# Kernel optimization log

Measured on AMD Instinct MI355X. Metric: run time of the kernel, lower is better.

The kernel has to match this reference:

```python
import jax, jax.numpy as jnp
import numpy as np

D_MODEL = 1024
N_HEADS = 16
HEAD_DIM = D_MODEL // N_HEADS


def setup_inputs() -> dict:
    key = jax.random.key(0)
    ks = jax.random.split(key, 10)
    B, NQ, S = 8, 64, 4096
    inv = 1.0 / np.sqrt(D_MODEL)
    inp = {
        "queries": jax.random.normal(ks[0], (B, NQ, D_MODEL), dtype=jnp.float32),
        "context": jax.random.normal(ks[1], (B, S, D_MODEL), dtype=jnp.float32),
        "wq": jax.random.normal(ks[2], (D_MODEL, D_MODEL), dtype=jnp.float32) * inv,
        "bq": jnp.zeros((D_MODEL,), dtype=jnp.float32),
        "wk": jax.random.normal(ks[3], (D_MODEL, D_MODEL), dtype=jnp.float32) * inv,
        "bk": jnp.zeros((D_MODEL,), dtype=jnp.float32),
        "wv": jax.random.normal(ks[4], (D_MODEL, D_MODEL), dtype=jnp.float32) * inv,
        "bv": jnp.zeros((D_MODEL,), dtype=jnp.float32),
        "wo": jax.random.normal(ks[5], (D_MODEL, D_MODEL), dtype=jnp.float32) * inv,
        "bo": jnp.zeros((D_MODEL,), dtype=jnp.float32),
    }
    return inp


def reference(queries, context, wq, bq, wk, bk, wv, bv, wo, bo):
    B, NQ, D = queries.shape
    S = context.shape[1]
    H, HD = N_HEADS, HEAD_DIM
    scale = HD ** -0.5
    # projections (x @ W^T + b, matching nn.Linear)
    q = queries @ wq.T + bq            # (B, NQ, D)
    k = context @ wk.T + bk            # (B, S, D)
    v = context @ wv.T + bv            # (B, S, D)
    q = q.reshape(B, NQ, H, HD).transpose(0, 2, 1, 3)  # (B, H, NQ, HD)
    k = k.reshape(B, S, H, HD).transpose(0, 2, 1, 3)   # (B, H, S, HD)
    v = v.reshape(B, S, H, HD).transpose(0, 2, 1, 3)   # (B, H, S, HD)
    attn = jnp.einsum('bhnd,bhsd->bhns', q, k) * scale
    attn = jax.nn.softmax(attn, axis=-1)
    # dropout is identity at eval / p=0
    out = jnp.einsum('bhns,bhsd->bhnd', attn, v)        # (B, H, NQ, HD)
    out = out.transpose(0, 2, 1, 3).reshape(B, NQ, D)   # (B, NQ, D)
    return out @ wo.T + bo
```

## Files before the change

### kernel.cpp

```cpp
#include <hip/hip_runtime.h>
#include <stdint.h>

#define BATCH   8
#define NQL     64
#define SLEN    4096
#define DMODEL  1024
#define NHEADS  16
#define HDIM    64

typedef float          f32x4  __attribute__((ext_vector_type(4)));
typedef __bf16         bf16x8 __attribute__((ext_vector_type(8)));
typedef unsigned int   u32x4  __attribute__((ext_vector_type(4)));
typedef unsigned short u16x4  __attribute__((ext_vector_type(4)));
typedef unsigned short u16x8  __attribute__((ext_vector_type(8)));

__device__ __forceinline__ unsigned short f2bf(float f) {
  unsigned int u = __builtin_bit_cast(unsigned int, f);
  u += 0x7FFFu + ((u >> 16) & 1u);
  return (unsigned short)(u >> 16);
}

__device__ __forceinline__ f32x4 mfma16(bf16x8 a, bf16x8 b, f32x4 c) {
  return __builtin_amdgcn_mfma_f32_16x16x32_bf16(a, b, c, 0, 0, 0);
}

__device__ __forceinline__ bf16x8 lds_frag(const char* p) {
  u32x4 v = *(const u32x4*)p;
  return __builtin_bit_cast(bf16x8, v);
}

__device__ __forceinline__ void gload_lds16(const void* g, void* l) {
  __builtin_amdgcn_global_load_lds((const __attribute__((address_space(1))) void*)g,
                                   (__attribute__((address_space(3))) void*)l, 16, 0, 0);
}

__global__ __launch_bounds__(256) void cvt_bf16_kernel(const float* __restrict__ in,
                                                       unsigned short* __restrict__ out,
                                                       int n8) {
  int i = blockIdx.x * 256 + threadIdx.x;
  if (i >= n8) return;
  const float4* p = (const float4*)in + (size_t)i * 2;
  float4 a = p[0], b = p[1];
  u16x8 o;
  o[0] = f2bf(a.x); o[1] = f2bf(a.y); o[2] = f2bf(a.z); o[3] = f2bf(a.w);
  o[4] = f2bf(b.x); o[5] = f2bf(b.y); o[6] = f2bf(b.z); o[7] = f2bf(b.w);
  *((u16x8*)out + i) = o;
}

template<int MODE>
__global__ __launch_bounds__(256)
void gemm_bt(const unsigned short* __restrict__ A, const unsigned short* __restrict__ Bw,
             const float* __restrict__ bias, void* __restrict__ Cout,
             int M, int N, int K) {
  __shared__ char lds[32768];
  char* ldsA = lds;
  char* ldsB = lds + 16384;

  const int tid  = threadIdx.x;
  const int wave = tid >> 6, lane = tid & 63;
  const int g    = lane >> 4, ln = lane & 15;
  const int nbn  = N >> 7;
  const int brow = (int)(blockIdx.x / nbn) << 7;
  const int bcol = (int)(blockIdx.x % nbn) << 7;
  const int wr   = wave >> 1, wc = wave & 1;

  f32x4 acc[4][4];
#pragma unroll
  for (int i = 0; i < 4; ++i)
#pragma unroll
    for (int j = 0; j < 4; ++j) acc[i][j] = (f32x4){0.f, 0.f, 0.f, 0.f};

  const int KT = K >> 6;
  const int srow = lane >> 3;
  const int srcs = (lane & 7) ^ (srow & 7);

  for (int kt = 0; kt < KT; ++kt) {
#pragma unroll
    for (int c = wave; c < 16; c += 4) {
      int row = (c << 3) + srow;
      const char* ga = (const char*)A + (((size_t)(brow + row) * K + (kt << 6) + (srcs << 3)) << 1);
      gload_lds16(ga, ldsA + (c << 10));
      const char* gb = (const char*)Bw + (((size_t)(bcol + row) * K + (kt << 6) + (srcs << 3)) << 1);
      gload_lds16(gb, ldsB + (c << 10));
    }
    asm volatile("s_waitcnt vmcnt(0)" ::: "memory");
    __syncthreads();

#pragma unroll
    for (int ks = 0; ks < 2; ++ks) {
      bf16x8 af[4], bfr[4];
      const int slot = ((ks << 2) + g) ^ (ln & 7);
#pragma unroll
      for (int mt = 0; mt < 4; ++mt) {
        int row = wr * 64 + mt * 16 + ln;
        af[mt] = lds_frag(ldsA + row * 128 + (slot << 4));
      }
#pragma unroll
      for (int nt = 0; nt < 4; ++nt) {
        int row = wc * 64 + nt * 16 + ln;
        bfr[nt] = lds_frag(ldsB + row * 128 + (slot << 4));
      }
#pragma unroll
      for (int mt = 0; mt < 4; ++mt)
#pragma unroll
        for (int nt = 0; nt < 4; ++nt)
          acc[mt][nt] = mfma16(af[mt], bfr[nt], acc[mt][nt]);
    }
    __syncthreads();
  }

#pragma unroll
  for (int mt = 0; mt < 4; ++mt) {
#pragma unroll
    for (int nt = 0; nt < 4; ++nt) {
      f32x4 v = acc[mt][nt];
      int r0 = brow + wr * 64 + mt * 16 + g * 4;
      int c  = bcol + wc * 64 + nt * 16 + ln;
      float bi = bias[c];
      if constexpr (MODE == 0) {
        unsigned short* Cb = (unsigned short*)Cout;
#pragma unroll
        for (int j = 0; j < 4; ++j) Cb[(size_t)(r0 + j) * N + c] = f2bf(v[j] + bi);
      } else if constexpr (MODE == 1) {
        float* Cf = (float*)Cout;
#pragma unroll
        for (int j = 0; j < 4; ++j) Cf[(size_t)(r0 + j) * N + c] = v[j] + bi;
      } else {
        u16x4 pk;
#pragma unroll
        for (int j = 0; j < 4; ++j) pk[j] = f2bf(v[j] + bi);
        size_t base = ((size_t)(r0 >> 12) * 1024 + c) * 4096 + (size_t)(r0 & 4095);
        *(u16x4*)((unsigned short*)Cout + base) = pk;
      }
    }
  }
}

__global__ __launch_bounds__(256)
void attn_kernel(const unsigned short* __restrict__ Qp,
                 const unsigned short* __restrict__ Kp,
                 const unsigned short* __restrict__ Vt,
                 unsigned short* __restrict__ Aout) {
  __shared__ char ldsKV[2][16384];
  __shared__ unsigned int plds[4 * 16 * 36];

  const int bh = blockIdx.x;
  const int b = bh >> 4, h = bh & 15;
  const int tid = threadIdx.x;
  const int wave = tid >> 6, lane = tid & 63;
  const int g = lane >> 4, ln = lane & 15;
  const int pbase = wave * 576 + ln * 36;
  const int srow = lane >> 3;
  const int srcs = (lane & 7) ^ (srow & 7);

  const unsigned short* qb =
      Qp + ((size_t)(b * 64 + wave * 16 + ln) * 1024) + h * 64 + g * 8;
  bf16x8 qf[2];
  qf[0] = __builtin_bit_cast(bf16x8, *(const u32x4*)qb);
  qf[1] = __builtin_bit_cast(bf16x8, *(const u32x4*)(qb + 32));

  f32x4 oacc[4];
#pragma unroll
  for (int i = 0; i < 4; ++i) oacc[i] = (f32x4){0.f, 0.f, 0.f, 0.f};
  float mrun = -1e30f, lrun = 0.f;

  auto stage = [&](int t, int buf) {
    int s0 = t << 6;
    char* bK = ldsKV[buf];
#pragma unroll
    for (int c4 = 0; c4 < 4; ++c4) {
      int c = wave * 4 + c4;
      int cc = c & 7;
      int row = (cc << 3) + srow;
      const char* gsrc;
      if (c < 8)
        gsrc = (const char*)Kp + (((size_t)((b << 12) + s0 + row) * 1024 + (h << 6) + (srcs << 3)) << 1);
      else
        gsrc = (const char*)Vt + (((size_t)((b << 10) + (h << 6) + row) * 4096 + s0 + (srcs << 3)) << 1);
      gload_lds16(gsrc, bK + ((c < 8) ? 0 : 8192) + (cc << 10));
    }
  };

  stage(0, 0);
  const int NT = SLEN / 64;
  for (int t = 0; t < NT; ++t) {
    asm volatile("s_waitcnt vmcnt(0)" ::: "memory");
    __syncthreads();
    if (t + 1 < NT) stage(t + 1, (t + 1) & 1);

    char* bufK = ldsKV[t & 1];
    char* bufV = bufK + 8192;

    f32x4 s4[4];
#pragma unroll
    for (int i = 0; i < 4; ++i) s4[i] = (f32x4){0.f, 0.f, 0.f, 0.f};
#pragma unroll
    for (int ks = 0; ks < 2; ++ks) {
      const int slot = ((ks << 2) + g) ^ (ln & 7);
#pragma unroll
      for (int mt = 0; mt < 4; ++mt) {
        int row = mt * 16 + ln;
        s4[mt] = mfma16(lds_frag(bufK + row * 128 + (slot << 4)), qf[ks], s4[mt]);
      }
    }

    float tmax = -1e30f;
#pragma unroll
    for (int mt = 0; mt < 4; ++mt)
#pragma unroll
      for (int j = 0; j < 4; ++j) {
        float sv = s4[mt][j] * 0.125f;
        s4[mt][j] = sv;
        tmax = fmaxf(tmax, sv);
      }
    tmax = fmaxf(tmax, __shfl_xor(tmax, 16));
    tmax = fmaxf(tmax, __shfl_xor(tmax, 32));
    float mnew = fmaxf(mrun, tmax);
    float factor = __expf(mrun - mnew);
    float psum = 0.f;
#pragma unroll
    for (int mt = 0; mt < 4; ++mt) {
      float p0 = __expf(s4[mt][0] - mnew);
      float p1 = __expf(s4[mt][1] - mnew);
      float p2 = __expf(s4[mt][2] - mnew);
      float p3 = __expf(s4[mt][3] - mnew);
      psum += (p0 + p1) + (p2 + p3);
      plds[pbase + mt * 8 + g * 2 + 0] = (unsigned)f2bf(p0) | ((unsigned)f2bf(p1) << 16);
      plds[pbase + mt * 8 + g * 2 + 1] = (unsigned)f2bf(p2) | ((unsigned)f2bf(p3) << 16);
    }
    psum += __shfl_xor(psum, 16);
    psum += __shfl_xor(psum, 32);
    lrun = lrun * factor + psum;
    mrun = mnew;

    float fj0 = __shfl(factor, g * 4 + 0);
    float fj1 = __shfl(factor, g * 4 + 1);
    float fj2 = __shfl(factor, g * 4 + 2);
    float fj3 = __shfl(factor, g * 4 + 3);
#pragma unroll
    for (int nt = 0; nt < 4; ++nt) {
      oacc[nt][0] *= fj0; oacc[nt][1] *= fj1; oacc[nt][2] *= fj2; oacc[nt][3] *= fj3;
    }

#pragma unroll
    for (int kt2 = 0; kt2 < 2; ++kt2) {
      u32x4 pv;
      int pidx = pbase + kt2 * 16 + g * 4;
      pv[0] = plds[pidx]; pv[1] = plds[pidx + 1]; pv[2] = plds[pidx + 2]; pv[3] = plds[pidx + 3];
      bf16x8 pa = __builtin_bit_cast(bf16x8, pv);
      const int slot = ((kt2 << 2) + g) ^ (ln & 7);
#pragma unroll
      for (int nt = 0; nt < 4; ++nt) {
        int row = nt * 16 + ln;
        oacc[nt] = mfma16(pa, lds_frag(bufV + row * 128 + (slot << 4)), oacc[nt]);
      }
    }
  }

  float l0 = __shfl(lrun, g * 4 + 0);
  float l1 = __shfl(lrun, g * 4 + 1);
  float l2 = __shfl(lrun, g * 4 + 2);
  float l3 = __shfl(lrun, g * 4 + 3);
  float r0 = 1.f / l0, r1 = 1.f / l1, r2 = 1.f / l2, r3 = 1.f / l3;
#pragma unroll
  for (int nt = 0; nt < 4; ++nt) {
    int col = h * 64 + nt * 16 + ln;
    size_t rbase = (size_t)(b * 64 + wave * 16 + g * 4) * 1024 + col;
    Aout[rbase + 0 * 1024] = f2bf(oacc[nt][0] * r0);
    Aout[rbase + 1 * 1024] = f2bf(oacc[nt][1] * r1);
    Aout[rbase + 2 * 1024] = f2bf(oacc[nt][2] * r2);
    Aout[rbase + 3 * 1024] = f2bf(oacc[nt][3] * r3);
  }
}

extern "C" void kernel_launch(void* const* d_in, const int* in_sizes, int n_in,
                              void* d_out, int out_size, void* d_ws, size_t ws_size,
                              hipStream_t stream) {
  const float* queries = (const float*)d_in[0];
  const float* context = (const float*)d_in[1];
  const float* wq = (const float*)d_in[2];
  const float* bq = (const float*)d_in[3];
  const float* wk = (const float*)d_in[4];
  const float* bk = (const float*)d_in[5];
  const float* wv = (const float*)d_in[6];
  const float* bv = (const float*)d_in[7];
  const float* wo = (const float*)d_in[8];
  const float* bo = (const float*)d_in[9];

  const size_t CTX_E = (size_t)BATCH * SLEN * DMODEL;
  const size_t QRY_E = (size_t)BATCH * NQL * DMODEL;
  const size_t W_E   = (size_t)DMODEL * DMODEL;

  char* ws = (char*)d_ws;
  size_t off = 0;
  auto alloc = [&](size_t bytes) {
    char* p = ws + off;
    off += (bytes + 255) & ~(size_t)255;
    return p;
  };
  unsigned short* ctx_bf = (unsigned short*)alloc(CTX_E * 2);
  unsigned short* q_bf   = (unsigned short*)alloc(QRY_E * 2);
  unsigned short* wq_bf  = (unsigned short*)alloc(W_E * 2);
  unsigned short* wk_bf  = (unsigned short*)alloc(W_E * 2);
  unsigned short* wv_bf  = (unsigned short*)alloc(W_E * 2);
  unsigned short* wo_bf  = (unsigned short*)alloc(W_E * 2);
  unsigned short* Qp     = (unsigned short*)alloc(QRY_E * 2);
  unsigned short* Kp     = (unsigned short*)alloc(CTX_E * 2);
  unsigned short* Vt     = (unsigned short*)alloc(CTX_E * 2);
  unsigned short* Ao     = (unsigned short*)alloc(QRY_E * 2);
  if (off > ws_size) return;

  cvt_bf16_kernel<<<dim3((int)(CTX_E / 8 / 256)), 256, 0, stream>>>(context, ctx_bf, (int)(CTX_E / 8));
  cvt_bf16_kernel<<<dim3((int)(QRY_E / 8 / 256)), 256, 0, stream>>>(queries, q_bf, (int)(QRY_E / 8));
  cvt_bf16_kernel<<<dim3((int)(W_E / 8 / 256)), 256, 0, stream>>>(wq, wq_bf, (int)(W_E / 8));
  cvt_bf16_kernel<<<dim3((int)(W_E / 8 / 256)), 256, 0, stream>>>(wk, wk_bf, (int)(W_E / 8));
  cvt_bf16_kernel<<<dim3((int)(W_E / 8 / 256)), 256, 0, stream>>>(wv, wv_bf, (int)(W_E / 8));
  cvt_bf16_kernel<<<dim3((int)(W_E / 8 / 256)), 256, 0, stream>>>(wo, wo_bf, (int)(W_E / 8));

  const int M_KV = BATCH * SLEN;
  const int M_Q  = BATCH * NQL;

  gemm_bt<0><<<dim3((M_KV / 128) * (DMODEL / 128)), 256, 0, stream>>>(ctx_bf, wk_bf, bk, Kp, M_KV, DMODEL, DMODEL);
  gemm_bt<2><<<dim3((M_KV / 128) * (DMODEL / 128)), 256, 0, stream>>>(ctx_bf, wv_bf, bv, Vt, M_KV, DMODEL, DMODEL);
  gemm_bt<0><<<dim3((M_Q / 128) * (DMODEL / 128)), 256, 0, stream>>>(q_bf, wq_bf, bq, Qp, M_Q, DMODEL, DMODEL);

  attn_kernel<<<dim3(BATCH * NHEADS), 256, 0, stream>>>(Qp, Kp, Vt, Ao);

  gemm_bt<1><<<dim3((M_Q / 128) * (DMODEL / 128)), 256, 0, stream>>>(Ao, wo_bf, bo, d_out, M_Q, DMODEL, DMODEL);
}
```

Before: 532.1 us.

## Add 256x256-tile triple-buffered GEMM for K/V projections with 32x32 MFMA

Adds a new GEMM kernel with 256x256 block tiles, 512 threads, 32x32x16 bf16 MFMA, a three-stage LDS ring buffer loaded directly from global memory, XOR-swizzled LDS addressing and an XCD-aware block remap. It is used for the large K and V projections, aiming for more data reuse per tile and better overlap of loads with compute. It also wraps the MFMA sections of the existing GEMM and attention kernels in s_setprio raises. Risks are higher register and LDS pressure (96KB LDS) and fewer blocks in flight.

After: 510.5 us. 1.04x faster.

```diff
diff --git a/kernel.cpp b/kernel.cpp
--- a/kernel.cpp
+++ b/kernel.cpp
@@ -9,6 +9,7 @@
 #define HDIM    64
 
 typedef float          f32x4  __attribute__((ext_vector_type(4)));
+typedef float          f32x16 __attribute__((ext_vector_type(16)));
 typedef __bf16         bf16x8 __attribute__((ext_vector_type(8)));
 typedef unsigned int   u32x4  __attribute__((ext_vector_type(4)));
 typedef unsigned short u16x4  __attribute__((ext_vector_type(4)));
@@ -47,6 +48,150 @@
   *((u16x8*)out + i) = o;
 }
 
+#define GF(a) ((a) ^ (((((a) >> 7) & 3) << 4) | ((((a) >> 9) & 1) << 6)))
+
+template<int MODE>
+__global__ __launch_bounds__(512, 2)
+void gemm256(const unsigned short* __restrict__ A, const unsigned short* __restrict__ Bw,
+             const float* __restrict__ bias, void* __restrict__ Cout,
+             int M, int N, int K) {
+  __shared__ char lds[98304];
+
+  const int tid = threadIdx.x;
+  const int wid = tid >> 6, lane = tid & 63;
+  const int l31 = lane & 31, lhi = lane >> 5;
+  const int wm = wid >> 2, wn = wid & 3;
+
+  const int nbn = N >> 8;
+  const int cpx = (int)gridDim.x >> 3;
+  const int bid = (int)blockIdx.x;
+  const int wg  = (bid & 7) * cpx + (bid >> 3);
+  const int brow = (wg / nbn) << 8;
+  const int bcol = (wg % nbn) << 8;
+
+  const int dA0 = wid * 1024 + lane * 16;
+  const int dA1 = dA0 + 8192;
+  const int a0 = GF(dA0), a1 = GF(dA1);
+  const int r0s = a0 >> 6, g0 = (a0 >> 4) & 3;
+  const int r1s = a1 >> 6, g1 = (a1 >> 4) & 3;
+  const unsigned short* srcA0 = A + (size_t)(brow + r0s) * K + g0 * 8;
+  const unsigned short* srcA1 = A + (size_t)(brow + r1s) * K + g1 * 8;
+  const unsigned short* srcB0 = Bw + (size_t)(bcol + r0s) * K + g0 * 8;
+  const unsigned short* srcB1 = Bw + (size_t)(bcol + r1s) * K + g1 * 8;
+  const int db0 = wid * 1024;
+  const int db1 = db0 + 8192;
+
+  int offA[4][2], offB[2][2];
+#pragma unroll
+  for (int mi = 0; mi < 4; ++mi)
+#pragma unroll
+    for (int ks = 0; ks < 2; ++ks) {
+      int r = wm * 128 + mi * 32 + l31;
+      int a = r * 64 + ks * 32 + lhi * 16;
+      offA[mi][ks] = GF(a);
+    }
+#pragma unroll
+  for (int ni = 0; ni < 2; ++ni)
+#pragma unroll
+    for (int ks = 0; ks < 2; ++ks) {
+      int r = wn * 64 + ni * 32 + l31;
+      int a = r * 64 + ks * 32 + lhi * 16;
+      offB[ni][ks] = GF(a) + 16384;
+    }
+
+  f32x16 acc[4][2];
+#pragma unroll
+  for (int mi = 0; mi < 4; ++mi)
+#pragma unroll
+    for (int ni = 0; ni < 2; ++ni)
+#pragma unroll
+      for (int e = 0; e < 16; ++e) acc[mi][ni][e] = 0.f;
+
+  auto stage = [&](int kt, int bo) {
+    const int ko = kt << 5;
+    char* base = lds + bo;
+    gload_lds16(srcA0 + ko, base + db0);
+    gload_lds16(srcA1 + ko, base + db1);
+    gload_lds16(srcB0 + ko, base + 16384 + db0);
+    gload_lds16(srcB1 + ko, base + 16384 + db1);
+  };
+
+  const int KT = K >> 5;
+  stage(0, 0);
+  stage(1, 32768);
+  asm volatile("s_waitcnt vmcnt(4)" ::: "memory");
+  __builtin_amdgcn_s_barrier();
+  __builtin_amdgcn_sched_barrier(0);
+
+  int bo = 0;
+  for (int kt = 0; kt < KT; ++kt) {
+    const bool st = (kt + 2 < KT);
+    if (st) {
+      int bo2 = bo + 65536;
+      if (bo2 >= 98304) bo2 -= 98304;
+      stage(kt + 2, bo2);
+    }
+    const char* bA = lds + bo;
+    bf16x8 af[4][2], bfr[2][2];
+#pragma unroll
+    for (int mi = 0; mi < 4; ++mi)
+#pragma unroll
+      for (int ks = 0; ks < 2; ++ks) af[mi][ks] = lds_frag(bA + offA[mi][ks]);
+#pragma unroll
+    for (int ni = 0; ni < 2; ++ni)
+#pragma unroll
+      for (int ks = 0; ks < 2; ++ks) bfr[ni][ks] = lds_frag(bA + offB[ni][ks]);
+
+    __builtin_amdgcn_s_setprio(1);
+#pragma unroll
+    for (int ks = 0; ks < 2; ++ks)
+#pragma unroll
+      for (int mi = 0; mi < 4; ++mi)
+#pragma unroll
+        for (int ni = 0; ni < 2; ++ni)
+          acc[mi][ni] = __builtin_amdgcn_mfma_f32_32x32x16_bf16(af[mi][ks], bfr[ni][ks],
+                                                                acc[mi][ni], 0, 0, 0);
+    __builtin_amdgcn_s_setprio(0);
+
+    if (kt + 1 < KT) {
+      if (st) asm volatile("s_waitcnt vmcnt(4)" ::: "memory");
+      else    asm volatile("s_waitcnt vmcnt(0)" ::: "memory");
+      __builtin_amdgcn_s_barrier();
+      __builtin_amdgcn_sched_barrier(0);
+    }
+    bo = (bo == 65536) ? 0 : bo + 32768;
+  }
+
+#pragma unroll
+  for (int mi = 0; mi < 4; ++mi) {
+#pragma unroll
+    for (int ni = 0; ni < 2; ++ni) {
+      f32x16 v = acc[mi][ni];
+      const int c = bcol + wn * 64 + ni * 32 + l31;
+      const float bi = bias[c];
+      const int rbase = brow + wm * 128 + mi * 32 + lhi * 4;
+      if constexpr (MODE == 0) {
+        unsigned short* Cb = (unsigned short*)Cout;
+#pragma unroll
+        for (int q = 0; q < 4; ++q)
+#pragma unroll
+          for (int j = 0; j < 4; ++j)
+            Cb[(size_t)(rbase + q * 8 + j) * N + c] = f2bf(v[q * 4 + j] + bi);
+      } else {
+        unsigned short* Vt = (unsigned short*)Cout;
+        const size_t fb = ((size_t)(rbase >> 12) * 1024 + c) * 4096;
+#pragma unroll
+        for (int q = 0; q < 4; ++q) {
+          u16x4 pk;
+#pragma unroll
+          for (int j = 0; j < 4; ++j) pk[j] = f2bf(v[q * 4 + j] + bi);
+          *(u16x4*)(Vt + fb + ((rbase + q * 8) & 4095)) = pk;
+        }
+      }
+    }
+  }
+}
+
 template<int MODE>
 __global__ __launch_bounds__(256)
 void gemm_bt(const unsigned short* __restrict__ A, const unsigned short* __restrict__ Bw,
@@ -100,11 +245,13 @@
         int row = wc * 64 + nt * 16 + ln;
         bfr[nt] = lds_frag(ldsB + row * 128 + (slot << 4));
       }
+      __builtin_amdgcn_s_setprio(1);
 #pragma unroll
       for (int mt = 0; mt < 4; ++mt)
 #pragma unroll
         for (int nt = 0; nt < 4; ++nt)
           acc[mt][nt] = mfma16(af[mt], bfr[nt], acc[mt][nt]);
+      __builtin_amdgcn_s_setprio(0);
     }
     __syncthreads();
   }
@@ -121,16 +268,10 @@
         unsigned short* Cb = (unsigned short*)Cout;
 #pragma unroll
         for (int j = 0; j < 4; ++j) Cb[(size_t)(r0 + j) * N + c] = f2bf(v[j] + bi);
-      } else if constexpr (MODE == 1) {
+      } else {
         float* Cf = (float*)Cout;
 #pragma unroll
         for (int j = 0; j < 4; ++j) Cf[(size_t)(r0 + j) * N + c] = v[j] + bi;
-      } else {
-        u16x4 pk;
-#pragma unroll
-        for (int j = 0; j < 4; ++j) pk[j] = f2bf(v[j] + bi);
-        size_t base = ((size_t)(r0 >> 12) * 1024 + c) * 4096 + (size_t)(r0 & 4095);
-        *(u16x4*)((unsigned short*)Cout + base) = pk;
       }
     }
   }
@@ -194,6 +335,7 @@
     f32x4 s4[4];
 #pragma unroll
     for (int i = 0; i < 4; ++i) s4[i] = (f32x4){0.f, 0.f, 0.f, 0.f};
+    __builtin_amdgcn_s_setprio(1);
 #pragma unroll
     for (int ks = 0; ks < 2; ++ks) {
       const int slot = ((ks << 2) + g) ^ (ln & 7);
@@ -203,6 +345,7 @@
         s4[mt] = mfma16(lds_frag(bufK + row * 128 + (slot << 4)), qf[ks], s4[mt]);
       }
     }
+    __builtin_amdgcn_s_setprio(0);
 
     float tmax = -1e30f;
 #pragma unroll
@@ -242,6 +385,7 @@
       oacc[nt][0] *= fj0; oacc[nt][1] *= fj1; oacc[nt][2] *= fj2; oacc[nt][3] *= fj3;
     }
 
+    __builtin_amdgcn_s_setprio(1);
 #pragma unroll
     for (int kt2 = 0; kt2 < 2; ++kt2) {
       u32x4 pv;
@@ -255,6 +399,7 @@
         oacc[nt] = mfma16(pa, lds_frag(bufV + row * 128 + (slot << 4)), oacc[nt]);
       }
     }
+    __builtin_amdgcn_s_setprio(0);
   }
 
   float l0 = __shfl(lrun, g * 4 + 0);
@@ -320,8 +465,9 @@
   const int M_KV = BATCH * SLEN;
   const int M_Q  = BATCH * NQL;
 
-  gemm_bt<0><<<dim3((M_KV / 128) * (DMODEL / 128)), 256, 0, stream>>>(ctx_bf, wk_bf, bk, Kp, M_KV, DMODEL, DMODEL);
-  gemm_bt<2><<<dim3((M_KV / 128) * (DMODEL / 128)), 256, 0, stream>>>(ctx_bf, wv_bf, bv, Vt, M_KV, DMODEL, DMODEL);
+  gemm256<0><<<dim3((M_KV / 256) * (DMODEL / 256)), 512, 0, stream>>>(ctx_bf, wk_bf, bk, Kp, M_KV, DMODEL, DMODEL);
+  gemm256<2><<<dim3((M_KV / 256) * (DMODEL / 256)), 512, 0, stream>>>(ctx_bf, wv_bf, bv, Vt, M_KV, DMODEL, DMODEL);
+
   gemm_bt<0><<<dim3((M_Q / 128) * (DMODEL / 128)), 256, 0, stream>>>(q_bf, wq_bf, bq, Qp, M_Q, DMODEL, DMODEL);
 
   attn_kernel<<<dim3(BATCH * NHEADS), 256, 0, stream>>>(Qp, Kp, Vt, Ao);
```
